# Performance work log

Measured on AMD Instinct MI355X. Metric: run time of the kernel, lower is better.

## Reference

```python
import jax, jax.numpy as jnp
import numpy as np

BINS = 32  # position_bins


def setup_inputs() -> dict:
    key = jax.random.key(0)
    ks = jax.random.split(key, 7)
    N, IN, E = 1024, 21, 128
    return {
        "target_feat": jax.random.normal(ks[0], (N, IN), dtype=jnp.float32),
        "residue_index": jnp.arange(N, dtype=jnp.int64),
        "Wa": jax.random.normal(ks[1], (E, IN), dtype=jnp.float32) * 0.1,
        "ba": jax.random.normal(ks[2], (E,), dtype=jnp.float32) * 0.1,
        "Wb": jax.random.normal(ks[3], (E, IN), dtype=jnp.float32) * 0.1,
        "bb": jax.random.normal(ks[4], (E,), dtype=jnp.float32) * 0.1,
        "Wp": jax.random.normal(ks[5], (E, 2 * BINS + 1), dtype=jnp.float32) * 0.1,
        "bp": jax.random.normal(ks[6], (E,), dtype=jnp.float32) * 0.1,
    }


def reference(target_feat, residue_index, Wa, ba, Wb, bb, Wp, bp):
    # Linear projections: [N, E]
    a = target_feat @ Wa.T + ba
    b = target_feat @ Wb.T + bb
    # Relative position bucket: [N, N] int in [0, 2*BINS]
    d = residue_index[:, None] - residue_index[None, :]
    d = jnp.clip(d, -BINS, BINS) + BINS
    # one_hot(d) @ Wp.T + bp  ==  row gather from Wp.T (fused, no one-hot)
    p = jnp.take(Wp.T, d, axis=0) + bp  # [N, N, E]
    # Outer broadcast sum z = a_i + b_j plus position term
    return a[:, None, :] + b[None, :, :] + p
```

## Files before the change

### kernel.cpp

```cpp
#include <hip/hip_runtime.h>

#define NN   1024
#define INF  21
#define EE   128
#define NB   65
#define BINSV 32

__global__ __launch_bounds__(128) void proj_kernel(
    const float* __restrict__ tf,
    const float* __restrict__ Wa, const float* __restrict__ ba,
    const float* __restrict__ Wb, const float* __restrict__ bb,
    float* __restrict__ a, float* __restrict__ b) {
  int i = blockIdx.x;
  int e = threadIdx.x;
  __shared__ float row[INF];
  if (e < INF) row[e] = tf[i * INF + e];
  __syncthreads();
  float sa = ba[e];
  float sb = bb[e];
#pragma unroll
  for (int k = 0; k < INF; ++k) {
    float r = row[k];
    sa = fmaf(r, Wa[e * INF + k], sa);
    sb = fmaf(r, Wb[e * INF + k], sb);
  }
  a[i * EE + e] = sa;
  b[i * EE + e] = sb;
}

__global__ __launch_bounds__(128) void ptab_kernel(
    const float* __restrict__ Wp, const float* __restrict__ bp,
    float* __restrict__ ptab) {
  int d = blockIdx.x;
  int e = threadIdx.x;
  ptab[d * EE + e] = Wp[e * NB + d] + bp[e];
}

__global__ __launch_bounds__(512) void fill_kernel(
    const float* __restrict__ a, const float* __restrict__ b,
    const float* __restrict__ ptab, const int* __restrict__ ri,
    float* __restrict__ out) {
  __shared__ int sri[NN];
  for (int t = threadIdx.x; t < NN; t += 512) sri[t] = ri[t];
  __syncthreads();

  const int i  = blockIdx.x;
  const int e4 = threadIdx.x & 31;
  const int jg = threadIdx.x >> 5;

  const float4 av = reinterpret_cast<const float4*>(a + i * EE)[e4];
  const int rii = sri[i];
  float4* outrow = reinterpret_cast<float4*>(out + (size_t)i * NN * EE);

  for (int j = jg; j < NN; j += 16) {
    int d = rii - sri[j];
    d = (d < -BINSV) ? -BINSV : (d > BINSV ? BINSV : d);
    d += BINSV;
    const float4 bv = reinterpret_cast<const float4*>(b + j * EE)[e4];
    const float4 pv = reinterpret_cast<const float4*>(ptab + d * EE)[e4];
    float4 o;
    o.x = av.x + bv.x + pv.x;
    o.y = av.y + bv.y + pv.y;
    o.z = av.z + bv.z + pv.z;
    o.w = av.w + bv.w + pv.w;
    outrow[j * 32 + e4] = o;
  }
}

extern "C" void kernel_launch(void* const* d_in, const int* in_sizes, int n_in,
                              void* d_out, int out_size, void* d_ws, size_t ws_size,
                              hipStream_t stream) {
  const float* tf = (const float*)d_in[0];
  const int*   ri = (const int*)d_in[1];
  const float* Wa = (const float*)d_in[2];
  const float* ba = (const float*)d_in[3];
  const float* Wb = (const float*)d_in[4];
  const float* bb = (const float*)d_in[5];
  const float* Wp = (const float*)d_in[6];
  const float* bp = (const float*)d_in[7];
  float* out = (float*)d_out;

  float* ws   = (float*)d_ws;
  float* a    = ws;
  float* b    = ws + NN * EE;
  float* ptab = ws + 2 * NN * EE;

  proj_kernel<<<NN, 128, 0, stream>>>(tf, Wa, ba, Wb, bb, a, b);
  ptab_kernel<<<NB, 128, 0, stream>>>(Wp, bp, ptab);
  fill_kernel<<<NN, 512, 0, stream>>>(a, b, ptab, ri, out);
}
```

Before: 111.7 us.

## Merge prep kernels, software-prefetch loads, and use nontemporal stores in fill

The projection and position-table kernels become one launch, with block index selecting the role, which removes one kernel launch. The fill loop now loads the next row's b and ptab vectors before storing the current output, overlapping load latency with stores. Output writes use nontemporal stores so the 512 MB output does not pollute the cache. The prefetch adds some register pressure, and nontemporal stores can behave differently depending on the hardware's write-combining.

```diff
diff --git a/kernel.cpp b/kernel.cpp
--- a/kernel.cpp
+++ b/kernel.cpp
@@ -6,34 +6,34 @@
 #define NB   65
 #define BINSV 32
 
-__global__ __launch_bounds__(128) void proj_kernel(
+typedef float f32x4 __attribute__((ext_vector_type(4)));
+
+__global__ __launch_bounds__(128) void prep_kernel(
     const float* __restrict__ tf,
     const float* __restrict__ Wa, const float* __restrict__ ba,
     const float* __restrict__ Wb, const float* __restrict__ bb,
-    float* __restrict__ a, float* __restrict__ b) {
-  int i = blockIdx.x;
-  int e = threadIdx.x;
-  __shared__ float row[INF];
-  if (e < INF) row[e] = tf[i * INF + e];
-  __syncthreads();
-  float sa = ba[e];
-  float sb = bb[e];
+    const float* __restrict__ Wp, const float* __restrict__ bp,
+    float* __restrict__ a, float* __restrict__ b, float* __restrict__ ptab) {
+  const int e = threadIdx.x;
+  if (blockIdx.x < NN) {
+    const int i = blockIdx.x;
+    __shared__ float row[INF];
+    if (e < INF) row[e] = tf[i * INF + e];
+    __syncthreads();
+    float sa = ba[e];
+    float sb = bb[e];
 #pragma unroll
-  for (int k = 0; k < INF; ++k) {
-    float r = row[k];
-    sa = fmaf(r, Wa[e * INF + k], sa);
-    sb = fmaf(r, Wb[e * INF + k], sb);
+    for (int k = 0; k < INF; ++k) {
+      float r = row[k];
+      sa = fmaf(r, Wa[e * INF + k], sa);
+      sb = fmaf(r, Wb[e * INF + k], sb);
+    }
+    a[i * EE + e] = sa;
+    b[i * EE + e] = sb;
+  } else {
+    const int d = blockIdx.x - NN;
+    ptab[d * EE + e] = Wp[e * NB + d] + bp[e];
   }
-  a[i * EE + e] = sa;
-  b[i * EE + e] = sb;
-}
-
-__global__ __launch_bounds__(128) void ptab_kernel(
-    const float* __restrict__ Wp, const float* __restrict__ bp,
-    float* __restrict__ ptab) {
-  int d = blockIdx.x;
-  int e = threadIdx.x;
-  ptab[d * EE + e] = Wp[e * NB + d] + bp[e];
 }
 
 __global__ __launch_bounds__(512) void fill_kernel(
@@ -48,23 +48,32 @@
   const int e4 = threadIdx.x & 31;
   const int jg = threadIdx.x >> 5;
 
-  const float4 av = reinterpret_cast<const float4*>(a + i * EE)[e4];
+  const f32x4* __restrict__ b4 = reinterpret_cast<const f32x4*>(b);
+  const f32x4* __restrict__ p4 = reinterpret_cast<const f32x4*>(ptab);
+
+  const f32x4 av = reinterpret_cast<const f32x4*>(a + i * EE)[e4];
   const int rii = sri[i];
-  float4* outrow = reinterpret_cast<float4*>(out + (size_t)i * NN * EE);
+  f32x4* outrow = reinterpret_cast<f32x4*>(out + (size_t)i * NN * EE);
 
-  for (int j = jg; j < NN; j += 16) {
+  auto bin = [&](int j) {
     int d = rii - sri[j];
     d = (d < -BINSV) ? -BINSV : (d > BINSV ? BINSV : d);
-    d += BINSV;
-    const float4 bv = reinterpret_cast<const float4*>(b + j * EE)[e4];
-    const float4 pv = reinterpret_cast<const float4*>(ptab + d * EE)[e4];
-    float4 o;
-    o.x = av.x + bv.x + pv.x;
-    o.y = av.y + bv.y + pv.y;
-    o.z = av.z + bv.z + pv.z;
-    o.w = av.w + bv.w + pv.w;
-    outrow[j * 32 + e4] = o;
+    return d + BINSV;
+  };
+
+  int j = jg;
+  f32x4 bv = b4[j * 32 + e4];
+  f32x4 pv = p4[bin(j) * 32 + e4];
+
+  for (int jn = jg + 16; jn < NN; jn += 16) {
+    f32x4 bvn = b4[jn * 32 + e4];
+    f32x4 pvn = p4[bin(jn) * 32 + e4];
+    f32x4 o = av + bv + pv;
+    __builtin_nontemporal_store(o, outrow + j * 32 + e4);
+    j = jn; bv = bvn; pv = pvn;
   }
+  f32x4 o = av + bv + pv;
+  __builtin_nontemporal_store(o, outrow + j * 32 + e4);
 }
 
 extern "C" void kernel_launch(void* const* d_in, const int* in_sizes, int n_in,
@@ -85,7 +94,6 @@
   float* b    = ws + NN * EE;
   float* ptab = ws + 2 * NN * EE;
 
-  proj_kernel<<<NN, 128, 0, stream>>>(tf, Wa, ba, Wb, bb, a, b);
-  ptab_kernel<<<NB, 128, 0, stream>>>(Wp, bp, ptab);
+  prep_kernel<<<NN + NB, 128, 0, stream>>>(tf, Wa, ba, Wb, bb, Wp, bp, a, b, ptab);
   fill_kernel<<<NN, 512, 0, stream>>>(a, b, ptab, ri, out);
 }
```

After: 109.8 us. About the same (-1.6%).
